# Optimization experiments

Hardware: AMD Instinct MI355X
Metric: run time of the kernel (lower is better)

Reference implementation:

```python
import jax, jax.numpy as jnp
import numpy as np

T, B, D, H, R, O = 32, 8, 512, 512, 32, 512
CLIP_VAL = 1.0
LN_EPS = 1e-5


def setup_inputs() -> dict:
    key = jax.random.key(0)
    ks = jax.random.split(key, 8)
    rn = lambda k, sh, sc: (jax.random.normal(k, sh) * sc).astype(jnp.float32)
    inp = {
        'x': rn(ks[0], (T, B, D), 1.0),
        'h0': jnp.zeros((B, H), jnp.float32),
        'v0': jnp.zeros((B, H), jnp.float32),
        'dU0': jnp.zeros((B, H, H), jnp.float32),
        'trace_e0': jnp.zeros((B, H), jnp.float32),
        'trace_E0': jnp.zeros((B, H, H), jnp.float32),
        # parameters (init-scale approximations of the torch inits)
        'x2h_w': rn(ks[1], (2 * H, D), 1.0 / np.sqrt(D)),
        'x2h_b': jnp.zeros((2 * H,), jnp.float32),
        'h2h_w': rn(ks[2], (2 * H, H), 1.0 / np.sqrt(H)),
        'h2h_b': jnp.zeros((2 * H,), jnp.float32),
        'lnx_g': jnp.ones((2 * H,), jnp.float32),
        'lnx_b': jnp.zeros((2 * H,), jnp.float32),
        'lnh_g': jnp.ones((2 * H,), jnp.float32),
        'lnh_b': jnp.zeros((2 * H,), jnp.float32),
        'h2mod_w': rn(ks[3], (R, H), np.sqrt(2.0 / H)),
        'h2mod_b': jnp.zeros((R,), jnp.float32),
        'mod2h_w': rn(ks[4], (3, R), np.sqrt(2.0 / R)),
        'mod2h_b': jnp.zeros((3,), jnp.float32),
        'alpha': jnp.full((1,), -4.0, jnp.float32),
        'tau_U': jnp.full((1,), -4.5, jnp.float32),
        'dec_w': rn(ks[5], (O, H), 1.0 / np.sqrt(H)),
        'dec_b': jnp.zeros((O,), jnp.float32),
    }
    return inp


def _ln(y, g, b):
    mu = jnp.mean(y, axis=-1, keepdims=True)
    yc = y - mu
    var = jnp.mean(yc * yc, axis=-1, keepdims=True)
    return g * yc * jax.lax.rsqrt(var + LN_EPS) + b


def reference(x, h0, v0, dU0, trace_e0, trace_E0,
              x2h_w, x2h_b, h2h_w, h2h_b,
              lnx_g, lnx_b, lnh_g, lnh_b,
              h2mod_w, h2mod_b, mod2h_w, mod2h_b,
              alpha, tau_U, dec_w, dec_b):
    Hh = h0.shape[-1]
    sp_alpha = jax.nn.softplus(alpha)            # (1,)
    tau = jax.nn.sigmoid(tau_U)                  # (1,)
    # clip bounds derived from the candidate-row block of h2h weight
    w_dv = h2h_w[Hh:2 * Hh]                      # [H, H]
    upper = jax.nn.relu(CLIP_VAL - w_dv) / (sp_alpha + 1e-8)
    lower = -jax.nn.relu(CLIP_VAL + w_dv) / (sp_alpha + 1e-8)

    def step(carry, xt):
        h, v, dU, te, tE = carry
        Wx = _ln(xt @ x2h_w.T + x2h_b, lnx_g, lnx_b)           # [B, 2H]
        Wh = h @ h2h_w.T + h2h_b                               # [B, 2H]
        plast = sp_alpha * jnp.einsum('bij,bj->bi', dU, h)     # [B, H]
        Wh = Wh.at[:, Hh:].add(plast)
        Wh = _ln(Wh, lnh_g, lnh_b)
        z, dv = jnp.split(Wx + Wh, 2, axis=-1)
        z = jax.nn.sigmoid(z)
        v_n = (1.0 - z) * v + z * dv
        nh = jax.nn.relu(v_n)
        mod = jax.nn.relu(nh @ h2mod_w.T + h2mod_b) @ mod2h_w.T + mod2h_b  # [B, 3]
        r = jax.nn.sigmoid(mod[:, :1])                          # [B, 1]
        s = jax.nn.sigmoid(mod[:, 1])[:, None, None]            # [B, 1, 1]
        m = mod[:, 2][:, None, None]                            # [B, 1, 1]
        te_n = (1.0 - r) * te + r * h
        outer = nh[:, :, None] * te_n[:, None, :]               # [B, H, H]
        tE_n = (1.0 - s) * tE + s * (outer - jnp.swapaxes(outer, 1, 2))
        dU_n = (1.0 - tau) * dU + tau * m * tE_n
        dU_n = jnp.where(dU_n > upper, upper, dU_n)
        dU_n = jnp.where(dU_n < lower, lower, dU_n)
        return (nh, v_n, dU_n, te_n, tE_n), nh

    carry0 = (h0, v0, dU0, trace_e0, trace_E0)
    _, hs = jax.lax.scan(step, carry0, x)                        # hs: [T, B, H]
    out = hs @ dec_w.T + dec_b                                   # [T, B, O]
    return out
```

## Files before the change

### kernel.cpp

```cpp
#include <hip/hip_runtime.h>

#define TT 32
#define BB 8
#define DD 512
#define HH 512
#define RR 32
#define OO 512
#define H2 1024

typedef unsigned int uint;
typedef float f32x2 __attribute__((ext_vector_type(2)));

#define OFF_WX    0
#define OFF_HS    262144
#define OFF_COLV  393216
#define OFF_TAGS  409600

#define HMW_P 528

__device__ __forceinline__ uint ld4_coh(const uint* p) {
  uint r;
  asm volatile("global_load_dword %0, %1, off sc0 sc1\n\ts_waitcnt vmcnt(0)"
               : "=v"(r) : "v"(p) : "memory");
  return r;
}
__device__ __forceinline__ f32x2 ld8_coh(const f32x2* p) {
  f32x2 r;
  asm volatile("global_load_dwordx2 %0, %1, off sc0 sc1\n\ts_waitcnt vmcnt(0)"
               : "=v"(r) : "v"(p) : "memory");
  return r;
}
__device__ __forceinline__ void st8_coh(f32x2* p, f32x2 v) {
  asm volatile("global_store_dwordx2 %0, %1, off sc0 sc1" :: "v"(p), "v"(v) : "memory");
}
__device__ __forceinline__ void st4_coh(uint* p, uint v) {
  asm volatile("global_store_dword %0, %1, off sc0 sc1" :: "v"(p), "v"(v) : "memory");
}
__device__ __forceinline__ float d4(const float4& a, const float4& b) {
  return a.x*b.x + a.y*b.y + a.z*b.z + a.w*b.w;
}

__global__ __launch_bounds__(512, 1) void sgru_persistent(
    const float* __restrict__ h0,     const float* __restrict__ v0,
    const float* __restrict__ dU0,    const float* __restrict__ tE0,
    const float* __restrict__ te0,
    const float* __restrict__ h2h_w,  const float* __restrict__ h2h_b,
    const float* __restrict__ lnh_g,  const float* __restrict__ lnh_b,
    const float* __restrict__ h2mod_w,const float* __restrict__ h2mod_b,
    const float* __restrict__ mod2h_w,const float* __restrict__ mod2h_b,
    const float* __restrict__ alpha_p,const float* __restrict__ tau_p,
    float* __restrict__ ws)
{
  const int tid = threadIdx.x;
  const int b   = blockIdx.x & 7;
  const int ir  = blockIdx.x >> 3;
  const int i0  = ir << 4;
  const int il  = tid >> 5;
  const int m   = tid & 31;
  const int gi  = i0 + il;

  const float* Wx = ws + OFF_WX;
  float* hsbuf    = ws + OFF_HS;
  f32x2* colvF    = (f32x2*)(ws + OFF_COLV);
  uint*  tagsP    = (uint*)(ws + OFF_TAGS);

  __shared__ float nh_s[2][HH];
  __shared__ float te_s[2][HH];
  __shared__ float hmw_s[RR * HMW_P];
  __shared__ float mp_s[RR];
  __shared__ float red_s[2][8];

  const float a_sp  = log1pf(__expf(alpha_p[0]));
  const float inv_a = 1.0f / (a_sp + 1e-8f);
  const float tau   = 1.0f / (1.0f + __expf(-tau_p[0]));
  const float c1t   = 1.0f - tau;

  float4 dUr[4], tEr[4], Wdvr[4], wlo[4], upr[4], lor[4];
  {
    const size_t rowoff = ((size_t)b * HH + gi) * HH;
    const size_t whioff = (size_t)(HH + gi) * HH;
    const size_t wlooff = (size_t)gi * HH;
#pragma unroll
    for (int q = 0; q < 4; ++q) {
      const int J = m + 32*q;
      dUr[q] = *reinterpret_cast<const float4*>(dU0 + rowoff + 4*J);
      tEr[q] = *reinterpret_cast<const float4*>(tE0 + rowoff + 4*J);
      wlo[q] = *reinterpret_cast<const float4*>(h2h_w + wlooff + 4*J);
      const float4 w = *reinterpret_cast<const float4*>(h2h_w + whioff + 4*J);
      Wdvr[q] = w;
      float4 u, l;
      u.x =  fmaxf(1.0f - w.x, 0.0f) * inv_a;  l.x = -fmaxf(1.0f + w.x, 0.0f) * inv_a;
      u.y =  fmaxf(1.0f - w.y, 0.0f) * inv_a;  l.y = -fmaxf(1.0f + w.y, 0.0f) * inv_a;
      u.z =  fmaxf(1.0f - w.z, 0.0f) * inv_a;  l.z = -fmaxf(1.0f + w.z, 0.0f) * inv_a;
      u.w =  fmaxf(1.0f - w.w, 0.0f) * inv_a;  l.w = -fmaxf(1.0f + w.w, 0.0f) * inv_a;
      upr[q] = u; lor[q] = l;
    }
  }

  const float rgz = lnh_g[tid],      rbz = lnh_b[tid];
  const float rgd = lnh_g[HH + tid], rbd = lnh_b[HH + tid];
  const float hbl = h2h_b[gi], hbh = h2h_b[HH + gi];
  const float hmb = h2mod_b[tid >> 4];
  const float mw0 = mod2h_w[tid & 31];
  const float mw1 = mod2h_w[RR + (tid & 31)];
  const float mw2 = mod2h_w[2*RR + (tid & 31)];
  const float mb0 = mod2h_b[0], mb1 = mod2h_b[1], mb2 = mod2h_b[2];
  float vreg = v0[b*HH + tid];

  nh_s[1][tid] = h0[b*HH + tid];
  te_s[0][tid] = te0[b*HH + tid];
  for (int idx = tid; idx < RR*HH; idx += 512)
    hmw_s[(idx >> 9)*HMW_P + (idx & 511)] = h2mod_w[idx];
  __syncthreads();

  {
    const float4* h4p = reinterpret_cast<const float4*>(nh_s[1]);
    float glo = 0.0f, gdv = 0.0f, plast = 0.0f;
#pragma unroll
    for (int q = 0; q < 4; ++q) {
      const float4 h4 = h4p[m + 32*q];
      glo   += d4(wlo[q],  h4);
      gdv   += d4(Wdvr[q], h4);
      plast += d4(dUr[q],  h4);
    }
#pragma unroll
    for (int off = 16; off >= 1; off >>= 1) {
      glo   += __shfl_xor(glo, off);
      gdv   += __shfl_xor(gdv, off);
      plast += __shfl_xor(plast, off);
    }
    if (m == 0) {
      f32x2 rec;
      rec.x = glo + hbl;
      rec.y = gdv + hbh + a_sp*plast;
      st8_coh(colvF + (size_t)(0*BB + b)*512 + gi, rec);
    }
    asm volatile("s_waitcnt vmcnt(0)" ::: "memory");
    __syncthreads();
    if (tid == 0) st4_coh(tagsP + (size_t)(0*BB + b)*32 + ir, 1u);
  }

  float wxz = Wx[(size_t)(0*BB + b)*H2 + tid];
  float wxd = Wx[(size_t)(0*BB + b)*H2 + HH + tid];

  for (int t = 0; t < TT; ++t) {
    const int cur = t & 1;
    const uint want = (uint)(t + 1);

    {
      const uint* tg = tagsP + (size_t)(cur*BB + b)*32;
      const int lane = tid & 63;
      for (;;) {
        uint v = want;
        if (lane < 32) v = ld4_coh(tg + lane);
        if (__all(v >= want)) break;
        __builtin_amdgcn_s_sleep(1);
      }
    }
    const f32x2 rec = ld8_coh(colvF + (size_t)(cur*BB + b)*512 + tid);
    const float whz = rec.x;
    const float whd = rec.y;

    float s1 = whz + whd, s2 = whz*whz + whd*whd;
#pragma unroll
    for (int off = 32; off >= 1; off >>= 1) {
      s1 += __shfl_xor(s1, off);
      s2 += __shfl_xor(s2, off);
    }
    if ((tid & 63) == 0) { red_s[0][tid >> 6] = s1; red_s[1][tid >> 6] = s2; }
    __syncthreads();
    s1 = 0.0f; s2 = 0.0f;
#pragma unroll
    for (int w = 0; w < 8; ++w) { s1 += red_s[0][w]; s2 += red_s[1][w]; }
    const float mu   = s1 * (1.0f / H2);
    const float var  = s2 * (1.0f / H2) - mu * mu;
    const float rstd = rsqrtf(var + 1e-5f);

    const float yz = (whz - mu)*rstd*rgz + rbz + wxz;
    const float yd = (whd - mu)*rstd*rgd + rbd + wxd;
    const float z  = 1.0f / (1.0f + __expf(-yz));
    vreg = vreg + z * (yd - vreg);
    const float nh = fmaxf(vreg, 0.0f);
    nh_s[cur][tid] = nh;
    if (ir == 0) hsbuf[(size_t)(t*BB + b)*HH + tid] = nh;
    if (t == TT - 1) return;

    wxz = Wx[(size_t)((t+1)*BB + b)*H2 + tid];
    wxd = Wx[(size_t)((t+1)*BB + b)*H2 + HH + tid];
    __syncthreads();

    float glo = 0.0f, gdv = 0.0f;
    float4 h4q[4];
    {
      const float4* nh4 = reinterpret_cast<const float4*>(nh_s[cur]);
#pragma unroll
      for (int q = 0; q < 4; ++q) {
        h4q[q] = nh4[m + 32*q];
        glo += d4(wlo[q],  h4q[q]);
        gdv += d4(Wdvr[q], h4q[q]);
      }
#pragma unroll
      for (int off = 16; off >= 1; off >>= 1) {
        glo += __shfl_xor(glo, off);
        gdv += __shfl_xor(gdv, off);
      }
    }
    {
      const int rr = tid >> 4, kk = tid & 15;
      float part = 0.0f;
#pragma unroll
      for (int j = 0; j < 32; ++j)
        part += hmw_s[rr*HMW_P + kk + 16*j] * nh_s[cur][kk + 16*j];
#pragma unroll
      for (int off = 8; off >= 1; off >>= 1) part += __shfl_xor(part, off);
      if (kk == 0) mp_s[rr] = fmaxf(part + hmb, 0.0f);
    }
    __syncthreads();

    float r_b, s_b, c2t;
    {
      const float mp = mp_s[tid & 31];
      float a0 = mw0*mp, a1 = mw1*mp, a2 = mw2*mp;
#pragma unroll
      for (int off = 16; off >= 1; off >>= 1) {
        a0 += __shfl_xor(a0, off);
        a1 += __shfl_xor(a1, off);
        a2 += __shfl_xor(a2, off);
      }
      r_b = 1.0f / (1.0f + __expf(-(a0 + mb0)));
      s_b = 1.0f / (1.0f + __expf(-(a1 + mb1)));
      c2t = tau * (a2 + mb2);
    }

    {
      const float teo = te_s[cur][tid];
      te_s[1 - cur][tid] = teo + r_b * (nh_s[1 - cur][tid] - teo);
    }

    const float nh_i  = nh_s[cur][gi];
    const float teo_i = te_s[cur][gi];
    const float hp_i  = nh_s[1 - cur][gi];
    const float te_i  = teo_i + r_b * (hp_i - teo_i);
    float plast = 0.0f;
    {
      const float4* te4o = reinterpret_cast<const float4*>(te_s[cur]);
      const float4* hp4  = reinterpret_cast<const float4*>(nh_s[1 - cur]);
#pragma unroll
      for (int q = 0; q < 4; ++q) {
        const int J = m + 32*q;
        const float4 h4 = h4q[q];
        const float4 to = te4o[J];
        const float4 hp = hp4[J];
#define SGRU_UPD(C) { \
        float ten = to.C + r_b * (hp.C - to.C);              \
        float o   = nh_i * ten - h4.C * te_i;                \
        float tEn = tEr[q].C + s_b * (o - tEr[q].C);         \
        tEr[q].C  = tEn;                                                             \
        float d   = c1t * dUr[q].C + c2t * tEn;              \
        d = fminf(d, upr[q].C); d = fmaxf(d, lor[q].C);      \
        dUr[q].C  = d;                                                               \
        plast = fmaf(d, h4.C, plast); }
        SGRU_UPD(x) SGRU_UPD(y) SGRU_UPD(z) SGRU_UPD(w)
#undef SGRU_UPD
      }
#pragma unroll
      for (int off = 16; off >= 1; off >>= 1) plast += __shfl_xor(plast, off);
    }

    if (m == 0) {
      f32x2 rec2;
      rec2.x = glo + hbl;
      rec2.y = gdv + hbh + a_sp*plast;
      st8_coh(colvF + (size_t)((1 - cur)*BB + b)*512 + gi, rec2);
    }
    asm volatile("s_waitcnt vmcnt(0)" ::: "memory");
    __syncthreads();
    if (tid == 0) st4_coh(tagsP + (size_t)((1 - cur)*BB + b)*32 + ir, (uint)(t + 2));
  }
}

#define GBM 32
#define GBN 32
#define GBK 32
__global__ __launch_bounds__(256) void gemm_tn(
    const float* __restrict__ A, const float* __restrict__ W,
    const float* __restrict__ bias, float* __restrict__ C,
    int M, int N)
{
  const int K = 512;
  const int nbn = N / GBN;
  const int m0 = (blockIdx.x / nbn) * GBM;
  const int n0 = (blockIdx.x % nbn) * GBN;
  const int tid = threadIdx.x;
  const int tx = tid & 15;
  const int ty = tid >> 4;
  const int lr = tid >> 3;
  const int lc = tid & 7;
  __shared__ float As[GBK][36];
  __shared__ float Ws[GBK][36];
  float acc[2][2] = {};
  for (int kc = 0; kc < K; kc += GBK) {
    const float4 a0 = *reinterpret_cast<const float4*>(A + (size_t)(m0 + lr)*K + kc + lc*4);
    const float4 w0 = *reinterpret_cast<const float4*>(W + (size_t)(n0 + lr)*K + kc + lc*4);
    __syncthreads();
    As[lc*4+0][lr] = a0.x; As[lc*4+1][lr] = a0.y; As[lc*4+2][lr] = a0.z; As[lc*4+3][lr] = a0.w;
    Ws[lc*4+0][lr] = w0.x; Ws[lc*4+1][lr] = w0.y; Ws[lc*4+2][lr] = w0.z; Ws[lc*4+3][lr] = w0.w;
    __syncthreads();
#pragma unroll
    for (int k = 0; k < GBK; ++k) {
      const float2 am = *reinterpret_cast<const float2*>(&As[k][ty*2]);
      const float2 wn = *reinterpret_cast<const float2*>(&Ws[k][tx*2]);
      acc[0][0] += am.x*wn.x; acc[0][1] += am.x*wn.y;
      acc[1][0] += am.y*wn.x; acc[1][1] += am.y*wn.y;
    }
  }
  const float b0 = bias[n0 + tx*2], b1 = bias[n0 + tx*2 + 1];
  C[(size_t)(m0 + ty*2 + 0)*N + n0 + tx*2]     = acc[0][0] + b0;
  C[(size_t)(m0 + ty*2 + 0)*N + n0 + tx*2 + 1] = acc[0][1] + b1;
  C[(size_t)(m0 + ty*2 + 1)*N + n0 + tx*2]     = acc[1][0] + b0;
  C[(size_t)(m0 + ty*2 + 1)*N + n0 + tx*2 + 1] = acc[1][1] + b1;
}

__global__ __launch_bounds__(256) void ln_apply(
    float* __restrict__ Wp, const float* __restrict__ g, const float* __restrict__ b,
    uint* __restrict__ tags)
{
  const int row = blockIdx.x;
  const int tid = threadIdx.x;
  if (row == 0) {
    tags[tid]       = 0u;
    tags[tid + 256] = 0u;
  }
  float* rp = Wp + (size_t)row * H2;
  float4 v = *reinterpret_cast<const float4*>(rp + tid*4);
  float s1 = v.x + v.y + v.z + v.w;
  float s2 = v.x*v.x + v.y*v.y + v.z*v.z + v.w*v.w;
#pragma unroll
  for (int off = 32; off >= 1; off >>= 1) {
    s1 += __shfl_xor(s1, off);
    s2 += __shfl_xor(s2, off);
  }
  __shared__ float red[2][4];
  if ((tid & 63) == 0) { red[0][tid >> 6] = s1; red[1][tid >> 6] = s2; }
  __syncthreads();
  s1 = red[0][0] + red[0][1] + red[0][2] + red[0][3];
  s2 = red[1][0] + red[1][1] + red[1][2] + red[1][3];
  const float mu   = s1 * (1.0f / H2);
  const float var  = s2 * (1.0f / H2) - mu * mu;
  const float rstd = rsqrtf(var + 1e-5f);
  const float4 gv = *reinterpret_cast<const float4*>(g + tid*4);
  const float4 bv = *reinterpret_cast<const float4*>(b + tid*4);
  v.x = gv.x*(v.x - mu)*rstd + bv.x;
  v.y = gv.y*(v.y - mu)*rstd + bv.y;
  v.z = gv.z*(v.z - mu)*rstd + bv.z;
  v.w = gv.w*(v.w - mu)*rstd + bv.w;
  *reinterpret_cast<float4*>(rp + tid*4) = v;
}

extern "C" void kernel_launch(void* const* d_in, const int* in_sizes, int n_in,
                              void* d_out, int out_size, void* d_ws, size_t ws_size,
                              hipStream_t stream) {
  (void)in_sizes; (void)n_in; (void)out_size; (void)ws_size;
  const float* x        = (const float*)d_in[0];
  const float* h0       = (const float*)d_in[1];
  const float* v0       = (const float*)d_in[2];
  const float* dU0      = (const float*)d_in[3];
  const float* te0      = (const float*)d_in[4];
  const float* tE0      = (const float*)d_in[5];
  const float* x2h_w    = (const float*)d_in[6];
  const float* x2h_b    = (const float*)d_in[7];
  const float* h2h_w    = (const float*)d_in[8];
  const float* h2h_b    = (const float*)d_in[9];
  const float* lnx_g    = (const float*)d_in[10];
  const float* lnx_b    = (const float*)d_in[11];
  const float* lnh_g    = (const float*)d_in[12];
  const float* lnh_b    = (const float*)d_in[13];
  const float* h2mod_w  = (const float*)d_in[14];
  const float* h2mod_b  = (const float*)d_in[15];
  const float* mod2h_w  = (const float*)d_in[16];
  const float* mod2h_b  = (const float*)d_in[17];
  const float* alpha    = (const float*)d_in[18];
  const float* tau_U    = (const float*)d_in[19];
  const float* dec_w    = (const float*)d_in[20];
  const float* dec_b    = (const float*)d_in[21];

  float* ws = (float*)d_ws;

  gemm_tn<<<(TT*BB/GBM) * (H2/GBN), 256, 0, stream>>>(x, x2h_w, x2h_b,
                                                      ws + OFF_WX, TT*BB, H2);
  ln_apply<<<TT*BB, 256, 0, stream>>>(ws + OFF_WX, lnx_g, lnx_b,
                                      (uint*)(ws + OFF_TAGS));

  sgru_persistent<<<256, 512, 0, stream>>>(h0, v0, dU0, tE0, te0,
                                           h2h_w, h2h_b, lnh_g, lnh_b,
                                           h2mod_w, h2mod_b, mod2h_w, mod2h_b,
                                           alpha, tau_U, ws);

  gemm_tn<<<(TT*BB/GBM) * (OO/GBN), 256, 0, stream>>>(ws + OFF_HS, dec_w, dec_b,
                                                      (float*)d_out, TT*BB, OO);
}
```

Before: 191.1 us.

## Pair two batches per block and replace per-block tag polling with atomic counters

Each persistent block now handles 8 rows for two batch elements (b and b+4), interleaving their steps so one batch's cross-block wait can overlap with the other's compute, and reuses the h2h weights across both batches. Per-block tag arrays that were polled by 32 lanes are replaced by a single atomic arrival counter per batch and parity, which cuts the global loads spent on synchronisation. Register use for dU/tE state stays about the same, but each block does twice the LN/mod work per step and the counters add atomic contention.

Result: slower. 328.5 us (+71.9%).

```diff
diff --git a/kernel.cpp b/kernel.cpp
--- a/kernel.cpp
+++ b/kernel.cpp
@@ -14,30 +14,213 @@
 #define OFF_WX    0
 #define OFF_HS    262144
 #define OFF_COLV  393216
-#define OFF_TAGS  409600
+#define OFF_CNT   409600
 
 #define HMW_P 528
 
-__device__ __forceinline__ uint ld4_coh(const uint* p) {
+__device__ __forceinline__ uint ld4_mall(const uint* p) {
   uint r;
   asm volatile("global_load_dword %0, %1, off sc0 sc1\n\ts_waitcnt vmcnt(0)"
                : "=v"(r) : "v"(p) : "memory");
   return r;
 }
-__device__ __forceinline__ f32x2 ld8_coh(const f32x2* p) {
+__device__ __forceinline__ f32x2 ld8_mall(const f32x2* p) {
   f32x2 r;
   asm volatile("global_load_dwordx2 %0, %1, off sc0 sc1\n\ts_waitcnt vmcnt(0)"
                : "=v"(r) : "v"(p) : "memory");
   return r;
 }
-__device__ __forceinline__ void st8_coh(f32x2* p, f32x2 v) {
+__device__ __forceinline__ void st8_mall(f32x2* p, f32x2 v) {
   asm volatile("global_store_dwordx2 %0, %1, off sc0 sc1" :: "v"(p), "v"(v) : "memory");
-}
-__device__ __forceinline__ void st4_coh(uint* p, uint v) {
-  asm volatile("global_store_dword %0, %1, off sc0 sc1" :: "v"(p), "v"(v) : "memory");
 }
 __device__ __forceinline__ float d4(const float4& a, const float4& b) {
   return a.x*b.x + a.y*b.y + a.z*b.z + a.w*b.w;
+}
+
+__device__ __forceinline__ void step_batch(
+    int t, int cur, int b, bool last,
+    int tid, int ir, int il, int m, int i0, int gi,
+    float4 (&dUr)[2], float4 (&tEr)[2], float& vreg, float& wxz, float& wxd,
+    const float4 (&wlo)[2], const float4 (&Wdvr)[2],
+    const float4 (&upr)[2], const float4 (&lor)[2],
+    float rgz, float rbz, float rgd, float rbd,
+    float hbl, float hbh, float hmb,
+    float mw0, float mw1, float mw2, float mb0, float mb1, float mb2,
+    float a_sp, float tau, float c1t,
+    float (*nh_s)[HH], float (*te_s)[HH],
+    const float* hmw_s, float* mp_s, float (*red_s)[8], f32x2* post_s,
+    const float* Wx, float* hsbuf, f32x2* colvF, uint* cnt)
+{
+  {
+    const uint want = 64u * ((uint)(t >> 1) + 1u);
+    if (tid < 64) {
+      const uint* cp = cnt + cur*BB + b;
+      for (;;) {
+        const uint v = ld4_mall(cp);
+        if (v >= want) break;
+        __builtin_amdgcn_s_sleep(1);
+      }
+    }
+    __syncthreads();
+  }
+  const f32x2 rec = ld8_mall(colvF + (size_t)(cur*BB + b)*512 + tid);
+  const float whz = rec.x, whd = rec.y;
+
+  float s1 = whz + whd, s2 = whz*whz + whd*whd;
+#pragma unroll
+  for (int off = 32; off >= 1; off >>= 1) {
+    s1 += __shfl_xor(s1, off);
+    s2 += __shfl_xor(s2, off);
+  }
+  if ((tid & 63) == 0) { red_s[0][tid >> 6] = s1; red_s[1][tid >> 6] = s2; }
+  __syncthreads();
+  s1 = 0.0f; s2 = 0.0f;
+#pragma unroll
+  for (int w = 0; w < 8; ++w) { s1 += red_s[0][w]; s2 += red_s[1][w]; }
+  const float mu   = s1 * (1.0f / H2);
+  const float var  = s2 * (1.0f / H2) - mu * mu;
+  const float rstd = rsqrtf(var + 1e-5f);
+
+  const float yz = (whz - mu)*rstd*rgz + rbz + wxz;
+  const float yd = (whd - mu)*rstd*rgd + rbd + wxd;
+  const float z  = 1.0f / (1.0f + __expf(-yz));
+  vreg = vreg + z * (yd - vreg);
+  const float nh = fmaxf(vreg, 0.0f);
+  nh_s[cur][tid] = nh;
+  if (ir == 0) hsbuf[(size_t)(t*BB + b)*HH + tid] = nh;
+  if (last) return;
+  __syncthreads();
+
+  float glo = 0.0f, gdv = 0.0f;
+  float4 h4q[2];
+  {
+    const float4* nh4 = reinterpret_cast<const float4*>(nh_s[cur]);
+#pragma unroll
+    for (int q = 0; q < 2; ++q) {
+      h4q[q] = nh4[m + 64*q];
+      glo += d4(wlo[q],  h4q[q]);
+      gdv += d4(Wdvr[q], h4q[q]);
+    }
+#pragma unroll
+    for (int off = 32; off >= 1; off >>= 1) {
+      glo += __shfl_xor(glo, off);
+      gdv += __shfl_xor(gdv, off);
+    }
+  }
+  {
+    const int rr = tid >> 4, kk = tid & 15;
+    float part = 0.0f;
+#pragma unroll
+    for (int j = 0; j < 32; ++j)
+      part += hmw_s[rr*HMW_P + kk + 16*j] * nh_s[cur][kk + 16*j];
+#pragma unroll
+    for (int off = 8; off >= 1; off >>= 1) part += __shfl_xor(part, off);
+    if (kk == 0) mp_s[rr] = fmaxf(part + hmb, 0.0f);
+  }
+  __syncthreads();
+
+  float r_b, s_b, c2t;
+  {
+    const float mp = mp_s[tid & 31];
+    float a0 = mw0*mp, a1 = mw1*mp, a2 = mw2*mp;
+#pragma unroll
+    for (int off = 16; off >= 1; off >>= 1) {
+      a0 += __shfl_xor(a0, off);
+      a1 += __shfl_xor(a1, off);
+      a2 += __shfl_xor(a2, off);
+    }
+    r_b = 1.0f / (1.0f + __expf(-(a0 + mb0)));
+    s_b = 1.0f / (1.0f + __expf(-(a1 + mb1)));
+    c2t = tau * (a2 + mb2);
+  }
+
+  {
+    const float teo = te_s[cur][tid];
+    te_s[1 - cur][tid] = teo + r_b * (nh_s[1 - cur][tid] - teo);
+  }
+
+  const float nh_i  = nh_s[cur][gi];
+  const float teo_i = te_s[cur][gi];
+  const float hp_i  = nh_s[1 - cur][gi];
+  const float te_i  = teo_i + r_b * (hp_i - teo_i);
+  float plast = 0.0f;
+  {
+    const float4* te4o = reinterpret_cast<const float4*>(te_s[cur]);
+    const float4* hp4  = reinterpret_cast<const float4*>(nh_s[1 - cur]);
+#pragma unroll
+    for (int q = 0; q < 2; ++q) {
+      const int J = m + 64*q;
+      const float4 h4 = h4q[q];
+      const float4 to = te4o[J];
+      const float4 hp = hp4[J];
+#define SGRU_UPD(C) { \
+      float ten = to.C + r_b * (hp.C - to.C);              \
+      float o   = nh_i * ten - h4.C * te_i;                \
+      float tEn = tEr[q].C + s_b * (o - tEr[q].C);         \
+      tEr[q].C  = tEn;                                                             \
+      float d   = c1t * dUr[q].C + c2t * tEn;              \
+      d = fminf(d, upr[q].C); d = fmaxf(d, lor[q].C);      \
+      dUr[q].C  = d;                                                               \
+      plast = fmaf(d, h4.C, plast); }
+      SGRU_UPD(x) SGRU_UPD(y) SGRU_UPD(z) SGRU_UPD(w)
+#undef SGRU_UPD
+    }
+#pragma unroll
+    for (int off = 32; off >= 1; off >>= 1) plast += __shfl_xor(plast, off);
+  }
+
+  if (m == 0) {
+    f32x2 pr;
+    pr.x = glo + hbl;
+    pr.y = gdv + hbh + a_sp*plast;
+    post_s[il] = pr;
+  }
+  __syncthreads();
+  if (tid < 64) {
+    if (tid < 8)
+      st8_mall(colvF + (size_t)((1 - cur)*BB + b)*512 + i0 + tid, post_s[tid]);
+    asm volatile("s_waitcnt vmcnt(0)" ::: "memory");
+    if (tid == 0) atomicAdd(cnt + (1 - cur)*BB + b, 1u);
+  }
+
+  wxz = Wx[(size_t)((t+1)*BB + b)*H2 + tid];
+  wxd = Wx[(size_t)((t+1)*BB + b)*H2 + HH + tid];
+}
+
+__device__ __forceinline__ void prologue_post(
+    int b, int tid, int il, int m, int i0,
+    const float4 (&dUr)[2], const float4 (&wlo)[2], const float4 (&Wdvr)[2],
+    float hbl, float hbh, float a_sp,
+    const float* nh1, f32x2* post_s, f32x2* colvF, uint* cnt)
+{
+  const float4* h4p = reinterpret_cast<const float4*>(nh1);
+  float glo = 0.0f, gdv = 0.0f, plast = 0.0f;
+#pragma unroll
+  for (int q = 0; q < 2; ++q) {
+    const float4 h4 = h4p[m + 64*q];
+    glo   += d4(wlo[q],  h4);
+    gdv   += d4(Wdvr[q], h4);
+    plast += d4(dUr[q],  h4);
+  }
+#pragma unroll
+  for (int off = 32; off >= 1; off >>= 1) {
+    glo   += __shfl_xor(glo, off);
+    gdv   += __shfl_xor(gdv, off);
+    plast += __shfl_xor(plast, off);
+  }
+  if (m == 0) {
+    f32x2 pr;
+    pr.x = glo + hbl;
+    pr.y = gdv + hbh + a_sp*plast;
+    post_s[il] = pr;
+  }
+  __syncthreads();
+  if (tid < 64) {
+    if (tid < 8)
+      st8_mall(colvF + (size_t)b*512 + i0 + tid, post_s[tid]);
+    asm volatile("s_waitcnt vmcnt(0)" ::: "memory");
+    if (tid == 0) atomicAdd(cnt + b, 1u);
+  }
 }
 
 __global__ __launch_bounds__(512, 1) void sgru_persistent(
@@ -52,39 +235,38 @@
     float* __restrict__ ws)
 {
   const int tid = threadIdx.x;
-  const int b   = blockIdx.x & 7;
-  const int ir  = blockIdx.x >> 3;
-  const int i0  = ir << 4;
-  const int il  = tid >> 5;
-  const int m   = tid & 31;
+  const int bgi = blockIdx.x & 3;
+  const int ir  = blockIdx.x >> 2;
+  const int b0  = bgi, b1 = bgi + 4;
+  const int i0  = ir << 3;
+  const int il  = tid >> 6;
+  const int m   = tid & 63;
   const int gi  = i0 + il;
 
   const float* Wx = ws + OFF_WX;
   float* hsbuf    = ws + OFF_HS;
   f32x2* colvF    = (f32x2*)(ws + OFF_COLV);
-  uint*  tagsP    = (uint*)(ws + OFF_TAGS);
-
-  __shared__ float nh_s[2][HH];
-  __shared__ float te_s[2][HH];
+  uint*  cnt      = (uint*)(ws + OFF_CNT);
+
+  __shared__ float nhA_s[2][HH], teA_s[2][HH];
+  __shared__ float nhB_s[2][HH], teB_s[2][HH];
   __shared__ float hmw_s[RR * HMW_P];
   __shared__ float mp_s[RR];
   __shared__ float red_s[2][8];
+  __shared__ f32x2 post_s[8];
 
   const float a_sp  = log1pf(__expf(alpha_p[0]));
   const float inv_a = 1.0f / (a_sp + 1e-8f);
   const float tau   = 1.0f / (1.0f + __expf(-tau_p[0]));
   const float c1t   = 1.0f - tau;
 
-  float4 dUr[4], tEr[4], Wdvr[4], wlo[4], upr[4], lor[4];
-  {
-    const size_t rowoff = ((size_t)b * HH + gi) * HH;
+  float4 wlo[2], Wdvr[2], upr[2], lor[2];
+  {
     const size_t whioff = (size_t)(HH + gi) * HH;
     const size_t wlooff = (size_t)gi * HH;
 #pragma unroll
-    for (int q = 0; q < 4; ++q) {
-      const int J = m + 32*q;
-      dUr[q] = *reinterpret_cast<const float4*>(dU0 + rowoff + 4*J);
-      tEr[q] = *reinterpret_cast<const float4*>(tE0 + rowoff + 4*J);
+    for (int q = 0; q < 2; ++q) {
+      const int J = m + 64*q;
       wlo[q] = *reinterpret_cast<const float4*>(h2h_w + wlooff + 4*J);
       const float4 w = *reinterpret_cast<const float4*>(h2h_w + whioff + 4*J);
       Wdvr[q] = w;
@@ -96,6 +278,19 @@
       upr[q] = u; lor[q] = l;
     }
   }
+  float4 dUrA[2], tErA[2], dUrB[2], tErB[2];
+  {
+    const size_t rowA = ((size_t)b0 * HH + gi) * HH;
+    const size_t rowB = ((size_t)b1 * HH + gi) * HH;
+#pragma unroll
+    for (int q = 0; q < 2; ++q) {
+      const int J = m + 64*q;
+      dUrA[q] = *reinterpret_cast<const float4*>(dU0 + rowA + 4*J);
+      tErA[q] = *reinterpret_cast<const float4*>(tE0 + rowA + 4*J);
+      dUrB[q] = *reinterpret_cast<const float4*>(dU0 + rowB + 4*J);
+      tErB[q] = *reinterpret_cast<const float4*>(tE0 + rowB + 4*J);
+    }
+  }
 
   const float rgz = lnh_g[tid],      rbz = lnh_b[tid];
   const float rgd = lnh_g[HH + tid], rbd = lnh_b[HH + tid];
@@ -105,177 +300,58 @@
   const float mw1 = mod2h_w[RR + (tid & 31)];
   const float mw2 = mod2h_w[2*RR + (tid & 31)];
   const float mb0 = mod2h_b[0], mb1 = mod2h_b[1], mb2 = mod2h_b[2];
-  float vreg = v0[b*HH + tid];
-
-  nh_s[1][tid] = h0[b*HH + tid];
-  te_s[0][tid] = te0[b*HH + tid];
+  float vregA = v0[b0*HH + tid];
+  float vregB = v0[b1*HH + tid];
+
+  nhA_s[1][tid] = h0[b0*HH + tid];
+  nhB_s[1][tid] = h0[b1*HH + tid];
+  teA_s[0][tid] = te0[b0*HH + tid];
+  teB_s[0][tid] = te0[b1*HH + tid];
   for (int idx = tid; idx < RR*HH; idx += 512)
     hmw_s[(idx >> 9)*HMW_P + (idx & 511)] = h2mod_w[idx];
   __syncthreads();
 
-  {
-    const float4* h4p = reinterpret_cast<const float4*>(nh_s[1]);
-    float glo = 0.0f, gdv = 0.0f, plast = 0.0f;
-#pragma unroll
-    for (int q = 0; q < 4; ++q) {
-      const float4 h4 = h4p[m + 32*q];
-      glo   += d4(wlo[q],  h4);
-      gdv   += d4(Wdvr[q], h4);
-      plast += d4(dUr[q],  h4);
-    }
-#pragma unroll
-    for (int off = 16; off >= 1; off >>= 1) {
-      glo   += __shfl_xor(glo, off);
-      gdv   += __shfl_xor(gdv, off);
-      plast += __shfl_xor(plast, off);
-    }
-    if (m == 0) {
-      f32x2 rec;
-      rec.x = glo + hbl;
-      rec.y = gdv + hbh + a_sp*plast;
-      st8_coh(colvF + (size_t)(0*BB + b)*512 + gi, rec);
-    }
-    asm volatile("s_waitcnt vmcnt(0)" ::: "memory");
-    __syncthreads();
-    if (tid == 0) st4_coh(tagsP + (size_t)(0*BB + b)*32 + ir, 1u);
-  }
-
-  float wxz = Wx[(size_t)(0*BB + b)*H2 + tid];
-  float wxd = Wx[(size_t)(0*BB + b)*H2 + HH + tid];
-
-  for (int t = 0; t < TT; ++t) {
+  prologue_post(b0, tid, il, m, i0, dUrA, wlo, Wdvr, hbl, hbh, a_sp,
+                nhA_s[1], post_s, colvF, cnt);
+  __syncthreads();
+  prologue_post(b1, tid, il, m, i0, dUrB, wlo, Wdvr, hbl, hbh, a_sp,
+                nhB_s[1], post_s, colvF, cnt);
+
+  float wxzA = Wx[(size_t)(0*BB + b0)*H2 + tid];
+  float wxdA = Wx[(size_t)(0*BB + b0)*H2 + HH + tid];
+  float wxzB = Wx[(size_t)(0*BB + b1)*H2 + tid];
+  float wxdB = Wx[(size_t)(0*BB + b1)*H2 + HH + tid];
+
+#pragma unroll 1
+  for (int t = 0; t < TT - 1; ++t) {
     const int cur = t & 1;
-    const uint want = (uint)(t + 1);
-
-    {
-      const uint* tg = tagsP + (size_t)(cur*BB + b)*32;
-      const int lane = tid & 63;
-      for (;;) {
-        uint v = want;
-        if (lane < 32) v = ld4_coh(tg + lane);
-        if (__all(v >= want)) break;
-        __builtin_amdgcn_s_sleep(1);
-      }
-    }
-    const f32x2 rec = ld8_coh(colvF + (size_t)(cur*BB + b)*512 + tid);
-    const float whz = rec.x;
-    const float whd = rec.y;
-
-    float s1 = whz + whd, s2 = whz*whz + whd*whd;
-#pragma unroll
-    for (int off = 32; off >= 1; off >>= 1) {
-      s1 += __shfl_xor(s1, off);
-      s2 += __shfl_xor(s2, off);
-    }
-    if ((tid & 63) == 0) { red_s[0][tid >> 6] = s1; red_s[1][tid >> 6] = s2; }
-    __syncthreads();
-    s1 = 0.0f; s2 = 0.0f;
-#pragma unroll
-    for (int w = 0; w < 8; ++w) { s1 += red_s[0][w]; s2 += red_s[1][w]; }
-    const float mu   = s1 * (1.0f / H2);
-    const float var  = s2 * (1.0f / H2) - mu * mu;
-    const float rstd = rsqrtf(var + 1e-5f);
-
-    const float yz = (whz - mu)*rstd*rgz + rbz + wxz;
-    const float yd = (whd - mu)*rstd*rgd + rbd + wxd;
-    const float z  = 1.0f / (1.0f + __expf(-yz));
-    vreg = vreg + z * (yd - vreg);
-    const float nh = fmaxf(vreg, 0.0f);
-    nh_s[cur][tid] = nh;
-    if (ir == 0) hsbuf[(size_t)(t*BB + b)*HH + tid] = nh;
-    if (t == TT - 1) return;
-
-    wxz = Wx[(size_t)((t+1)*BB + b)*H2 + tid];
-    wxd = Wx[(size_t)((t+1)*BB + b)*H2 + HH + tid];
-    __syncthreads();
-
-    float glo = 0.0f, gdv = 0.0f;
-    float4 h4q[4];
-    {
-      const float4* nh4 = reinterpret_cast<const float4*>(nh_s[cur]);
-#pragma unroll
-      for (int q = 0; q < 4; ++q) {
-        h4q[q] = nh4[m + 32*q];
-        glo += d4(wlo[q],  h4q[q]);
-        gdv += d4(Wdvr[q], h4q[q]);
-      }
-#pragma unroll
-      for (int off = 16; off >= 1; off >>= 1) {
-        glo += __shfl_xor(glo, off);
-        gdv += __shfl_xor(gdv, off);
-      }
-    }
-    {
-      const int rr = tid >> 4, kk = tid & 15;
-      float part = 0.0f;
-#pragma unroll
-      for (int j = 0; j < 32; ++j)
-        part += hmw_s[rr*HMW_P + kk + 16*j] * nh_s[cur][kk + 16*j];
-#pragma unroll
-      for (int off = 8; off >= 1; off >>= 1) part += __shfl_xor(part, off);
-      if (kk == 0) mp_s[rr] = fmaxf(part + hmb, 0.0f);
-    }
-    __syncthreads();
-
-    float r_b, s_b, c2t;
-    {
-      const float mp = mp_s[tid & 31];
-      float a0 = mw0*mp, a1 = mw1*mp, a2 = mw2*mp;
-#pragma unroll
-      for (int off = 16; off >= 1; off >>= 1) {
-        a0 += __shfl_xor(a0, off);
-        a1 += __shfl_xor(a1, off);
-        a2 += __shfl_xor(a2, off);
-      }
-      r_b = 1.0f / (1.0f + __expf(-(a0 + mb0)));
-      s_b = 1.0f / (1.0f + __expf(-(a1 + mb1)));
-      c2t = tau * (a2 + mb2);
-    }
-
-    {
-      const float teo = te_s[cur][tid];
-      te_s[1 - cur][tid] = teo + r_b * (nh_s[1 - cur][tid] - teo);
-    }
-
-    const float nh_i  = nh_s[cur][gi];
-    const float teo_i = te_s[cur][gi];
-    const float hp_i  = nh_s[1 - cur][gi];
-    const float te_i  = teo_i + r_b * (hp_i - teo_i);
-    float plast = 0.0f;
-    {
-      const float4* te4o = reinterpret_cast<const float4*>(te_s[cur]);
-      const float4* hp4  = reinterpret_cast<const float4*>(nh_s[1 - cur]);
-#pragma unroll
-      for (int q = 0; q < 4; ++q) {
-        const int J = m + 32*q;
-        const float4 h4 = h4q[q];
-        const float4 to = te4o[J];
-        const float4 hp = hp4[J];
-#define SGRU_UPD(C) { \
-        float ten = to.C + r_b * (hp.C - to.C);              \
-        float o   = nh_i * ten - h4.C * te_i;                \
-        float tEn = tEr[q].C + s_b * (o - tEr[q].C);         \
-        tEr[q].C  = tEn;                                                             \
-        float d   = c1t * dUr[q].C + c2t * tEn;              \
-        d = fminf(d, upr[q].C); d = fmaxf(d, lor[q].C);      \
-        dUr[q].C  = d;                                                               \
-        plast = fmaf(d, h4.C, plast); }
-        SGRU_UPD(x) SGRU_UPD(y) SGRU_UPD(z) SGRU_UPD(w)
-#undef SGRU_UPD
-      }
-#pragma unroll
-      for (int off = 16; off >= 1; off >>= 1) plast += __shfl_xor(plast, off);
-    }
-
-    if (m == 0) {
-      f32x2 rec2;
-      rec2.x = glo + hbl;
-      rec2.y = gdv + hbh + a_sp*plast;
-      st8_coh(colvF + (size_t)((1 - cur)*BB + b)*512 + gi, rec2);
-    }
-    asm volatile("s_waitcnt vmcnt(0)" ::: "memory");
-    __syncthreads();
-    if (tid == 0) st4_coh(tagsP + (size_t)((1 - cur)*BB + b)*32 + ir, (uint)(t + 2));
+    step_batch(t, cur, b0, false, tid, ir, il, m, i0, gi,
+               dUrA, tErA, vregA, wxzA, wxdA, wlo, Wdvr, upr, lor,
+               rgz, rbz, rgd, rbd, hbl, hbh, hmb,
+               mw0, mw1, mw2, mb0, mb1, mb2, a_sp, tau, c1t,
+               nhA_s, teA_s, hmw_s, mp_s, red_s, post_s,
+               Wx, hsbuf, colvF, cnt);
+    step_batch(t, cur, b1, false, tid, ir, il, m, i0, gi,
+               dUrB, tErB, vregB, wxzB, wxdB, wlo, Wdvr, upr, lor,
+               rgz, rbz, rgd, rbd, hbl, hbh, hmb,
+               mw0, mw1, mw2, mb0, mb1, mb2, a_sp, tau, c1t,
+               nhB_s, teB_s, hmw_s, mp_s, red_s, post_s,
+               Wx, hsbuf, colvF, cnt);
+  }
+  {
+    const int t = TT - 1, cur = t & 1;
+    step_batch(t, cur, b0, true, tid, ir, il, m, i0, gi,
+               dUrA, tErA, vregA, wxzA, wxdA, wlo, Wdvr, upr, lor,
+               rgz, rbz, rgd, rbd, hbl, hbh, hmb,
+               mw0, mw1, mw2, mb0, mb1, mb2, a_sp, tau, c1t,
+               nhA_s, teA_s, hmw_s, mp_s, red_s, post_s,
+               Wx, hsbuf, colvF, cnt);
+    step_batch(t, cur, b1, true, tid, ir, il, m, i0, gi,
+               dUrB, tErB, vregB, wxzB, wxdB, wlo, Wdvr, upr, lor,
+               rgz, rbz, rgd, rbd, hbl, hbh, hmb,
+               mw0, mw1, mw2, mb0, mb1, mb2, a_sp, tau, c1t,
+               nhB_s, teB_s, hmw_s, mp_s, red_s, post_s,
+               Wx, hsbuf, colvF, cnt);
   }
 }
 
@@ -323,14 +399,11 @@
 
 __global__ __launch_bounds__(256) void ln_apply(
     float* __restrict__ Wp, const float* __restrict__ g, const float* __restrict__ b,
-    uint* __restrict__ tags)
+    uint* __restrict__ cnt)
 {
   const int row = blockIdx.x;
   const int tid = threadIdx.x;
-  if (row == 0) {
-    tags[tid]       = 0u;
-    tags[tid + 256] = 0u;
-  }
+  if (row == 0 && tid < 16) cnt[tid] = 0u;
   float* rp = Wp + (size_t)row * H2;
   float4 v = *reinterpret_cast<const float4*>(rp + tid*4);
   float s1 = v.x + v.y + v.z + v.w;
@@ -389,7 +462,7 @@
   gemm_tn<<<(TT*BB/GBM) * (H2/GBN), 256, 0, stream>>>(x, x2h_w, x2h_b,
                                                       ws + OFF_WX, TT*BB, H2);
   ln_apply<<<TT*BB, 256, 0, stream>>>(ws + OFF_WX, lnx_g, lnx_b,
-                                      (uint*)(ws + OFF_TAGS));
+                                      (uint*)(ws + OFF_CNT));
 
   sgru_persistent<<<256, 512, 0, stream>>>(h0, v0, dU0, tE0, te0,
                                            h2h_w, h2h_b, lnh_g, lnh_b,
```

## Pack partial LN statistics into widened flags for cross-block step sync

Applied to the files above, without the earlier changes.

Each block now stages its 16 column values in shared memory and writes them with one wave. It then publishes a 16-byte flag that holds the step tag plus partial sums and sums of squares for the LayerNorm. Consumers poll these flags and reduce the statistics from them directly, so the block-wide reduction over the gathered column vector and one barrier are gone from the step's critical path. The cost is larger flag records and reliance on the two tag copies to detect a torn 16-byte write. Summation order also changes, which can shift results slightly in floating point.

New measurement: 197.2 us. 3.2% more time.

```diff
diff --git a/kernel.cpp b/kernel.cpp
--- a/kernel.cpp
+++ b/kernel.cpp
@@ -10,34 +10,57 @@
 
 typedef unsigned int uint;
 typedef float f32x2 __attribute__((ext_vector_type(2)));
+typedef uint  u32x4 __attribute__((ext_vector_type(4)));
 
 #define OFF_WX    0
 #define OFF_HS    262144
 #define OFF_COLV  393216
-#define OFF_TAGS  409600
+#define OFF_FLG   409600
 
 #define HMW_P 528
 
-__device__ __forceinline__ uint ld4_coh(const uint* p) {
-  uint r;
-  asm volatile("global_load_dword %0, %1, off sc0 sc1\n\ts_waitcnt vmcnt(0)"
-               : "=v"(r) : "v"(p) : "memory");
-  return r;
-}
-__device__ __forceinline__ f32x2 ld8_coh(const f32x2* p) {
+__device__ __forceinline__ f32x2 ld8_mall(const f32x2* p) {
   f32x2 r;
   asm volatile("global_load_dwordx2 %0, %1, off sc0 sc1\n\ts_waitcnt vmcnt(0)"
                : "=v"(r) : "v"(p) : "memory");
   return r;
 }
-__device__ __forceinline__ void st8_coh(f32x2* p, f32x2 v) {
+__device__ __forceinline__ void st8_mall(f32x2* p, f32x2 v) {
   asm volatile("global_store_dwordx2 %0, %1, off sc0 sc1" :: "v"(p), "v"(v) : "memory");
 }
-__device__ __forceinline__ void st4_coh(uint* p, uint v) {
-  asm volatile("global_store_dword %0, %1, off sc0 sc1" :: "v"(p), "v"(v) : "memory");
+__device__ __forceinline__ u32x4 ld16_mall(const u32x4* p) {
+  u32x4 r;
+  asm volatile("global_load_dwordx4 %0, %1, off sc0 sc1\n\ts_waitcnt vmcnt(0)"
+               : "=v"(r) : "v"(p) : "memory");
+  return r;
+}
+__device__ __forceinline__ void st16_mall(u32x4* p, u32x4 v) {
+  asm volatile("global_store_dwordx4 %0, %1, off sc0 sc1" :: "v"(p), "v"(v) : "memory");
 }
 __device__ __forceinline__ float d4(const float4& a, const float4& b) {
   return a.x*b.x + a.y*b.y + a.z*b.z + a.w*b.w;
+}
+
+__device__ __forceinline__ void post_flag(f32x2* colv_dst, u32x4* flag_dst,
+                                          uint tag, int tid, const f32x2* post_s) {
+  if (tid < 64) {
+    if (tid < 16) st8_mall(colv_dst + tid, post_s[tid]);
+    f32x2 pv;
+    pv.x = 0.0f; pv.y = 0.0f;
+    if (tid < 16) pv = post_s[tid];
+    float e1 = pv.x + pv.y, e2 = pv.x*pv.x + pv.y*pv.y;
+#pragma unroll
+    for (int off = 8; off >= 1; off >>= 1) {
+      e1 += __shfl_xor(e1, off);
+      e2 += __shfl_xor(e2, off);
+    }
+    asm volatile("s_waitcnt vmcnt(0)" ::: "memory");
+    if (tid == 0) {
+      u32x4 fr;
+      fr.x = tag; fr.y = __float_as_uint(e1); fr.z = __float_as_uint(e2); fr.w = tag;
+      st16_mall(flag_dst, fr);
+    }
+  }
 }
 
 __global__ __launch_bounds__(512, 1) void sgru_persistent(
@@ -62,13 +85,14 @@
   const float* Wx = ws + OFF_WX;
   float* hsbuf    = ws + OFF_HS;
   f32x2* colvF    = (f32x2*)(ws + OFF_COLV);
-  uint*  tagsP    = (uint*)(ws + OFF_TAGS);
+  u32x4* flags16  = (u32x4*)(ws + OFF_FLG);
 
   __shared__ float nh_s[2][HH];
   __shared__ float te_s[2][HH];
   __shared__ float hmw_s[RR * HMW_P];
   __shared__ float mp_s[RR];
-  __shared__ float red_s[2][8];
+  __shared__ float stat_s[2];
+  __shared__ f32x2 post_s[16];
 
   const float a_sp  = log1pf(__expf(alpha_p[0]));
   const float inv_a = 1.0f / (a_sp + 1e-8f);
@@ -130,14 +154,14 @@
       plast += __shfl_xor(plast, off);
     }
     if (m == 0) {
-      f32x2 rec;
-      rec.x = glo + hbl;
-      rec.y = gdv + hbh + a_sp*plast;
-      st8_coh(colvF + (size_t)(0*BB + b)*512 + gi, rec);
-    }
-    asm volatile("s_waitcnt vmcnt(0)" ::: "memory");
-    __syncthreads();
-    if (tid == 0) st4_coh(tagsP + (size_t)(0*BB + b)*32 + ir, 1u);
+      f32x2 pr;
+      pr.x = glo + hbl;
+      pr.y = gdv + hbh + a_sp*plast;
+      post_s[il] = pr;
+    }
+    __syncthreads();
+    post_flag(colvF + (size_t)(0*BB + b)*512 + i0,
+              flags16 + (size_t)(0*BB + b)*32 + ir, 1u, tid, post_s);
   }
 
   float wxz = Wx[(size_t)(0*BB + b)*H2 + tid];
@@ -147,37 +171,33 @@
     const int cur = t & 1;
     const uint want = (uint)(t + 1);
 
-    {
-      const uint* tg = tagsP + (size_t)(cur*BB + b)*32;
-      const int lane = tid & 63;
+    if (tid < 64) {
+      const u32x4* fp = flags16 + (size_t)(cur*BB + b)*32 + (tid & 31);
+      u32x4 f;
       for (;;) {
-        uint v = want;
-        if (lane < 32) v = ld4_coh(tg + lane);
-        if (__all(v >= want)) break;
+        f = ld16_mall(fp);
+        if (__all((f.x >= want) && (f.w >= want))) break;
         __builtin_amdgcn_s_sleep(1);
       }
-    }
-    const f32x2 rec = ld8_coh(colvF + (size_t)(cur*BB + b)*512 + tid);
-    const float whz = rec.x;
-    const float whd = rec.y;
-
-    float s1 = whz + whd, s2 = whz*whz + whd*whd;
-#pragma unroll
-    for (int off = 32; off >= 1; off >>= 1) {
-      s1 += __shfl_xor(s1, off);
-      s2 += __shfl_xor(s2, off);
-    }
-    if ((tid & 63) == 0) { red_s[0][tid >> 6] = s1; red_s[1][tid >> 6] = s2; }
-    __syncthreads();
-    s1 = 0.0f; s2 = 0.0f;
-#pragma unroll
-    for (int w = 0; w < 8; ++w) { s1 += red_s[0][w]; s2 += red_s[1][w]; }
-    const float mu   = s1 * (1.0f / H2);
-    const float var  = s2 * (1.0f / H2) - mu * mu;
-    const float rstd = rsqrtf(var + 1e-5f);
-
-    const float yz = (whz - mu)*rstd*rgz + rbz + wxz;
-    const float yd = (whd - mu)*rstd*rgd + rbd + wxd;
+      float s1 = __uint_as_float(f.y), s2 = __uint_as_float(f.z);
+#pragma unroll
+      for (int off = 16; off >= 1; off >>= 1) {
+        s1 += __shfl_xor(s1, off);
+        s2 += __shfl_xor(s2, off);
+      }
+      if (tid == 0) {
+        const float mu  = s1 * (1.0f / H2);
+        const float var = s2 * (1.0f / H2) - mu * mu;
+        stat_s[0] = mu;
+        stat_s[1] = rsqrtf(var + 1e-5f);
+      }
+    }
+    __syncthreads();
+
+    const f32x2 rec = ld8_mall(colvF + (size_t)(cur*BB + b)*512 + tid);
+    const float mu = stat_s[0], rstd = stat_s[1];
+    const float yz = (rec.x - mu)*rstd*rgz + rbz + wxz;
+    const float yd = (rec.y - mu)*rstd*rgd + rbd + wxd;
     const float z  = 1.0f / (1.0f + __expf(-yz));
     vreg = vreg + z * (yd - vreg);
     const float nh = fmaxf(vreg, 0.0f);
@@ -268,14 +288,14 @@
     }
 
     if (m == 0) {
-      f32x2 rec2;
-      rec2.x = glo + hbl;
-      rec2.y = gdv + hbh + a_sp*plast;
-      st8_coh(colvF + (size_t)((1 - cur)*BB + b)*512 + gi, rec2);
-    }
-    asm volatile("s_waitcnt vmcnt(0)" ::: "memory");
-    __syncthreads();
-    if (tid == 0) st4_coh(tagsP + (size_t)((1 - cur)*BB + b)*32 + ir, (uint)(t + 2));
+      f32x2 pr;
+      pr.x = glo + hbl;
+      pr.y = gdv + hbh + a_sp*plast;
+      post_s[il] = pr;
+    }
+    __syncthreads();
+    post_flag(colvF + (size_t)((1 - cur)*BB + b)*512 + i0,
+              flags16 + (size_t)((1 - cur)*BB + b)*32 + ir, (uint)(t + 2), tid, post_s);
   }
 }
 
@@ -323,13 +343,16 @@
 
 __global__ __launch_bounds__(256) void ln_apply(
     float* __restrict__ Wp, const float* __restrict__ g, const float* __restrict__ b,
-    uint* __restrict__ tags)
+    u32x4* __restrict__ flags16)
 {
   const int row = blockIdx.x;
   const int tid = threadIdx.x;
-  if (row == 0) {
-    tags[tid]       = 0u;
-    tags[tid + 256] = 0u;
+  {
+    const int idx = row * 256 + tid;
+    if (idx < 2*BB*32) {
+      u32x4 z; z.x = 0u; z.y = 0u; z.z = 0u; z.w = 0u;
+      flags16[idx] = z;
+    }
   }
   float* rp = Wp + (size_t)row * H2;
   float4 v = *reinterpret_cast<const float4*>(rp + tid*4);
@@ -389,7 +412,7 @@
   gemm_tn<<<(TT*BB/GBM) * (H2/GBN), 256, 0, stream>>>(x, x2h_w, x2h_b,
                                                       ws + OFF_WX, TT*BB, H2);
   ln_apply<<<TT*BB, 256, 0, stream>>>(ws + OFF_WX, lnx_g, lnx_b,
-                                      (uint*)(ws + OFF_TAGS));
+                                      (u32x4*)(ws + OFF_FLG));
 
   sgru_persistent<<<256, 512, 0, stream>>>(h0, v0, dU0, tE0, te0,
                                            h2h_w, h2h_b, lnh_g, lnh_b,
```
